# Kernel optimization log

Measured on AMD Instinct MI355X. Metric: run time of the kernel, lower is better.

Reference implementation:

```python
import jax, jax.numpy as jnp
import numpy as np

DIM = 1024
NUM_HEADS = 16
HEAD_DIM = DIM // NUM_HEADS
B, L = 4, 2048


def setup_inputs() -> dict:
    key = jax.random.key(0)
    ks = jax.random.split(key, 9)
    s = 0.02
    return {
        "x": jax.random.normal(ks[0], (B, L, DIM), jnp.float32),
        "Wq": jax.random.normal(ks[1], (DIM, DIM), jnp.float32) * s,
        "bq": jax.random.normal(ks[2], (DIM,), jnp.float32) * s,
        "Wk": jax.random.normal(ks[3], (DIM, DIM), jnp.float32) * s,
        "bk": jax.random.normal(ks[4], (DIM,), jnp.float32) * s,
        "Wv": jax.random.normal(ks[5], (DIM, DIM), jnp.float32) * s,
        "bv": jax.random.normal(ks[6], (DIM,), jnp.float32) * s,
        "Wo": jax.random.normal(ks[7], (DIM, DIM), jnp.float32) * s,
        "bo": jax.random.normal(ks[8], (DIM,), jnp.float32) * s,
    }


def _alibi_bias_causal(seq_len, dtype):
    # slopes m_h = 2^(-8h/H), h = 1..H
    h = jnp.arange(1, NUM_HEADS + 1, dtype=jnp.float32)
    slopes = jnp.power(2.0, -8.0 * h / NUM_HEADS)  # [H]
    pos = jnp.arange(seq_len, dtype=jnp.float32)
    rel = jnp.abs(pos[:, None] - pos[None, :])  # [L, L]
    bias = -slopes[:, None, None] * rel[None, :, :]  # [H, L, L]
    causal = pos[:, None] >= pos[None, :]  # lower-triangular True
    bias = jnp.where(causal[None, :, :], bias, -jnp.inf)
    return bias.astype(dtype)  # [H, L, L]


def reference(x, Wq, bq, Wk, bk, Wv, bv, Wo, bo):
    b, l, d = x.shape
    # torch Linear: y = x @ W.T + b
    q = (jnp.einsum('bld,ed->ble', x, Wq) + bq).reshape(b, l, NUM_HEADS, HEAD_DIM).transpose(0, 2, 1, 3)
    k = (jnp.einsum('bld,ed->ble', x, Wk) + bk).reshape(b, l, NUM_HEADS, HEAD_DIM).transpose(0, 2, 1, 3)
    v = (jnp.einsum('bld,ed->ble', x, Wv) + bv).reshape(b, l, NUM_HEADS, HEAD_DIM).transpose(0, 2, 1, 3)

    scale = 1.0 / np.sqrt(HEAD_DIM)
    scores = jnp.einsum('bhqd,bhkd->bhqk', q, k) * scale  # [B,H,L,L]
    scores = scores + _alibi_bias_causal(l, scores.dtype)[None]  # causal -inf inside bias
    attn = jax.nn.softmax(scores, axis=-1)
    out = jnp.einsum('bhqk,bhkd->bhqd', attn, v)  # [B,H,L,hd]
    out = out.transpose(0, 2, 1, 3).reshape(b, l, d)
    return jnp.einsum('bld,ed->ble', out, Wo) + bo
```

## Files before the change

### kernel.cpp

```cpp
#include <hip/hip_runtime.h>
#include <hip/hip_bf16.h>

typedef __bf16 bf16;
typedef __attribute__((ext_vector_type(4))) __bf16 bf16x4;
typedef __attribute__((ext_vector_type(8))) __bf16 bf16x8;
typedef __attribute__((ext_vector_type(4))) float f32x4;

#define MFMA16(a,b,c) __builtin_amdgcn_mfma_f32_16x16x32_bf16((a),(b),(c),0,0,0)

constexpr int BSZ = 4, SEQ = 2048, DIM = 1024, NH = 16, HD = 64;
constexpr long SZ    = (long)BSZ * SEQ * DIM;
constexpr long BSLOT = (long)SEQ * DIM;
constexpr long WSZ   = (long)DIM * DIM;

__device__ inline bf16x8 ld8(const bf16* p) { return *(const bf16x8*)p; }
__device__ inline bf16x8 ld8(const float* p) {
    f32x4 a = *(const f32x4*)p;
    f32x4 b = *(const f32x4*)(p + 4);
    bf16x8 r;
    r[0] = (bf16)a[0]; r[1] = (bf16)a[1]; r[2] = (bf16)a[2]; r[3] = (bf16)a[3];
    r[4] = (bf16)b[0]; r[5] = (bf16)b[1]; r[6] = (bf16)b[2]; r[7] = (bf16)b[3];
    return r;
}

__device__ inline void async16(const bf16* g, bf16* l) {
    __builtin_amdgcn_global_load_lds(
        (const __attribute__((address_space(1))) unsigned int*)g,
        (__attribute__((address_space(3))) unsigned int*)l,
        16, 0, 0);
}

__global__ __launch_bounds__(256) void cvt1(const float* __restrict__ s,
                                            bf16* __restrict__ d, long n) {
    const long i = ((long)blockIdx.x * 256 + threadIdx.x) * 8;
    if (i < n) *(bf16x8*)(d + i) = ld8(s + i);
}
__global__ __launch_bounds__(256) void cvt3(
    const float* __restrict__ s0, const float* __restrict__ s1, const float* __restrict__ s2,
    bf16* __restrict__ d0, bf16* __restrict__ d1, bf16* __restrict__ d2, long n) {
    const float* s = (blockIdx.z == 0) ? s0 : ((blockIdx.z == 1) ? s1 : s2);
    bf16* d        = (blockIdx.z == 0) ? d0 : ((blockIdx.z == 1) ? d1 : d2);
    const long i = ((long)blockIdx.x * 256 + threadIdx.x) * 8;
    if (i < n) *(bf16x8*)(d + i) = ld8(s + i);
}

template <typename CT>
__global__ __launch_bounds__(256) void gemm_bb(
    const bf16* __restrict__ A,
    const bf16* __restrict__ W0, const bf16* __restrict__ W1, const bf16* __restrict__ W2,
    const float* __restrict__ b0, const float* __restrict__ b1, const float* __restrict__ b2,
    CT* __restrict__ C0, CT* __restrict__ C1, CT* __restrict__ C2,
    int M, int N, int K)
{
    const int z = blockIdx.z;
    const bf16* W     = (z == 0) ? W0 : ((z == 1) ? W1 : W2);
    const float* bias = (z == 0) ? b0 : ((z == 1) ? b1 : b2);
    CT* C             = (z == 0) ? C0 : ((z == 1) ? C1 : C2);

    __shared__ __align__(16) bf16 As[128][32];
    __shared__ __align__(16) bf16 Bs[128][32];

    const int tid  = threadIdx.x;
    const int lane = tid & 63;
    const int wave = tid >> 6;
    const int l15  = lane & 15;
    const int quad = lane >> 4;

    const int m0 = blockIdx.x * 128;
    const int n0 = blockIdx.y * 128;
    const int wm = (wave >> 1) * 64;
    const int wn = (wave & 1) * 64;

    f32x4 acc[4][4];
#pragma unroll
    for (int i = 0; i < 4; i++)
#pragma unroll
        for (int j = 0; j < 4; j++) acc[i][j] = f32x4{0.f, 0.f, 0.f, 0.f};

    const int r1 = tid >> 2,         c1 = (tid & 3) * 8;
    const int r2 = (tid + 256) >> 2, c2 = ((tid + 256) & 3) * 8;

    for (int k0 = 0; k0 < K; k0 += 32) {
        __syncthreads();
        async16(A + (long)(m0 + r1) * K + k0 + c1, &As[r1][c1]);
        async16(A + (long)(m0 + r2) * K + k0 + c2, &As[r2][c2]);
        async16(W + (long)(n0 + r1) * K + k0 + c1, &Bs[r1][c1]);
        async16(W + (long)(n0 + r2) * K + k0 + c2, &Bs[r2][c2]);
        __syncthreads();

        bf16x8 af[4], bfr[4];
#pragma unroll
        for (int t = 0; t < 4; t++) {
            af[t]  = *(const bf16x8*)&As[wm + t * 16 + l15][quad * 8];
            bfr[t] = *(const bf16x8*)&Bs[wn + t * 16 + l15][quad * 8];
        }
#pragma unroll
        for (int i = 0; i < 4; i++)
#pragma unroll
            for (int j = 0; j < 4; j++)
                acc[i][j] = MFMA16(af[i], bfr[j], acc[i][j]);
    }

#pragma unroll
    for (int j = 0; j < 4; j++) {
        const float bv = bias[n0 + wn + j * 16 + l15];
        const long col = n0 + wn + j * 16 + l15;
#pragma unroll
        for (int i = 0; i < 4; i++) {
            const long row = m0 + wm + i * 16 + quad * 4;
#pragma unroll
            for (int r = 0; r < 4; r++)
                C[(row + r) * N + col] = (CT)(acc[i][j][r] + bv);
        }
    }
}

template <typename AT, typename CT>
__global__ __launch_bounds__(256) void gemm_bt(
    const AT* __restrict__ A,
    const float* __restrict__ W0, const float* __restrict__ W1, const float* __restrict__ W2,
    const float* __restrict__ b0, const float* __restrict__ b1, const float* __restrict__ b2,
    CT* __restrict__ C0, CT* __restrict__ C1, CT* __restrict__ C2,
    int M, int N, int K)
{
    const int z = blockIdx.z;
    const float* W    = (z == 0) ? W0 : ((z == 1) ? W1 : W2);
    const float* bias = (z == 0) ? b0 : ((z == 1) ? b1 : b2);
    CT* C             = (z == 0) ? C0 : ((z == 1) ? C1 : C2);

    __shared__ __align__(16) bf16 As[128][32];
    __shared__ __align__(16) bf16 Bs[128][32];

    const int tid  = threadIdx.x;
    const int lane = tid & 63;
    const int wave = tid >> 6;
    const int l15  = lane & 15;
    const int quad = lane >> 4;

    const int m0 = blockIdx.x * 128;
    const int n0 = blockIdx.y * 128;
    const int wm = (wave >> 1) * 64;
    const int wn = (wave & 1) * 64;

    f32x4 acc[4][4];
#pragma unroll
    for (int i = 0; i < 4; i++)
#pragma unroll
        for (int j = 0; j < 4; j++) acc[i][j] = f32x4{0.f, 0.f, 0.f, 0.f};

    const int r1 = tid >> 2,         c1 = (tid & 3) * 8;
    const int r2 = (tid + 256) >> 2, c2 = ((tid + 256) & 3) * 8;

    for (int k0 = 0; k0 < K; k0 += 32) {
        __syncthreads();
        *(bf16x8*)&As[r1][c1] = ld8(A + (long)(m0 + r1) * K + k0 + c1);
        *(bf16x8*)&As[r2][c2] = ld8(A + (long)(m0 + r2) * K + k0 + c2);
        *(bf16x8*)&Bs[r1][c1] = ld8(W + (long)(n0 + r1) * K + k0 + c1);
        *(bf16x8*)&Bs[r2][c2] = ld8(W + (long)(n0 + r2) * K + k0 + c2);
        __syncthreads();

        bf16x8 af[4], bfr[4];
#pragma unroll
        for (int t = 0; t < 4; t++) {
            af[t]  = *(const bf16x8*)&As[wm + t * 16 + l15][quad * 8];
            bfr[t] = *(const bf16x8*)&Bs[wn + t * 16 + l15][quad * 8];
        }
#pragma unroll
        for (int i = 0; i < 4; i++)
#pragma unroll
            for (int j = 0; j < 4; j++)
                acc[i][j] = MFMA16(af[i], bfr[j], acc[i][j]);
    }

#pragma unroll
    for (int j = 0; j < 4; j++) {
        const float bv = bias[n0 + wn + j * 16 + l15];
        const long col = n0 + wn + j * 16 + l15;
#pragma unroll
        for (int i = 0; i < 4; i++) {
            const long row = m0 + wm + i * 16 + quad * 4;
#pragma unroll
            for (int r = 0; r < 4; r++)
                C[(row + r) * N + col] = (CT)(acc[i][j][r] + bv);
        }
    }
}

__global__ __launch_bounds__(256, 4) void attn(
    const bf16* __restrict__ Kw, const bf16* __restrict__ Vw,
    bf16* __restrict__ QOw)
{
    const int z  = blockIdx.x;
    const int bh = blockIdx.y;
    const int b = bh >> 4, h = bh & 15;
    const int qtA = z, qtB = 31 - z;
    const int tid = threadIdx.x, wave = tid >> 6, lane = tid & 63;
    const int l15 = lane & 15, quad = lane >> 4;

    __shared__ __align__(16) bf16 Vt[2][64][72];
    __shared__ __align__(16) bf16 Pl[4][16][72];
    __shared__ __align__(16) bf16 Kt[2][64][64];

    const long base = (long)b * SEQ * DIM + h * HD;
    const int q0A = qtA * 64 + wave * 16;
    const int q0B = qtB * 64 + wave * 16;

    bf16x8 qA0, qA1, qB0, qB1;
    {
        const bf16* pA = QOw + base + (long)(q0A + l15) * DIM + quad * 8;
        qA0 = *(const bf16x8*)pA; qA1 = *(const bf16x8*)(pA + 32);
        const bf16* pB = QOw + base + (long)(q0B + l15) * DIM + quad * 8;
        qB0 = *(const bf16x8*)pB; qB1 = *(const bf16x8*)(pB + 32);
    }

    constexpr float LOG2E = 1.4426950408889634f;
    const float slope = exp2f(-0.5f * (float)(h + 1));
    const float c1 = 0.125f * LOG2E;
    const float ns = slope * LOG2E;
    const float MC = 16.0f * LOG2E;

    float lrA = 0.f, lrB = 0.f;
    f32x4 oA[4], oB[4];
#pragma unroll
    for (int d = 0; d < 4; d++) { oA[d] = f32x4{0,0,0,0}; oB[d] = f32x4{0,0,0,0}; }

    auto stageV = [&](int kt, int bi) {
#pragma unroll
        for (int t = 0; t < 2; t++) {
            const int s = tid + 256 * t;
            const int key = s >> 3, dg8 = (s & 7) * 8;
            bf16x8 v = *(const bf16x8*)(Vw + base + (long)(kt * 64 + key) * DIM + dg8);
            const int col = key ^ dg8;
#pragma unroll
            for (int i = 0; i < 8; i++) Vt[bi][dg8 + i][col] = v[i];
        }
    };

    auto stageK = [&](int kt, int bi) {
#pragma unroll
        for (int t = 0; t < 2; t++) {
            const int s = tid + 256 * t;
            const int r = s >> 3, u = s & 7;
            const int gc = (u ^ (r & 7)) * 8;
            async16(Kw + base + (long)(kt * 64 + r) * DIM + gc, &Kt[bi][r][u * 8]);
        }
    };

    stageK(0, 0);
    stageV(0, 0);
    __syncthreads();

    const int klq = quad * 4;
    const int qlB = wave * 16 + l15;
    const int kc0 = (quad ^ (l15 & 7)) * 8;

    for (int kt = 0; kt <= qtB; kt++) {
        const int bi = kt & 1;
        if (kt < qtB) { stageK(kt + 1, bi ^ 1); stageV(kt + 1, bi ^ 1); }
        const bool dual = (kt <= qtA);

        f32x4 sB[4], sA[4];
#pragma unroll
        for (int nt = 0; nt < 4; nt++) {
            const int row = nt * 16 + l15;
            bf16x8 k0 = *(const bf16x8*)&Kt[bi][row][kc0];
            bf16x8 k1 = *(const bf16x8*)&Kt[bi][row][kc0 ^ 32];
            f32x4 a = f32x4{0,0,0,0};
            a = MFMA16(k0, qB0, a); a = MFMA16(k1, qB1, a);
            sB[nt] = a;
            if (dual) {
                f32x4 c = f32x4{0,0,0,0};
                c = MFMA16(k0, qA0, c); c = MFMA16(k1, qA1, c);
                sA[nt] = c;
            }
        }

        {
            const float t0 = fmaf(ns, (float)(kt * 64 + klq - q0B - l15), -MC);
            const bool diag = (kt == qtB);
#pragma unroll
            for (int nt = 0; nt < 4; nt++) {
                const float bn = fmaf(ns, (float)(16 * nt), t0);
                bf16x4 p4;
#pragma unroll
                for (int r = 0; r < 4; r++) {
                    float arg = fmaf(sB[nt][r], c1, fmaf(ns, (float)r, bn));
                    if (diag && (nt * 16 + klq + r > qlB)) arg = -1e30f;
                    const float p = exp2f(arg);
                    lrB += p;
                    p4[r] = (bf16)p;
                }
                *(bf16x4*)&Pl[wave][l15][nt * 16 + klq] = p4;
            }
            bf16x8 p0 = *(const bf16x8*)&Pl[wave][l15][quad * 8];
            bf16x8 p1 = *(const bf16x8*)&Pl[wave][l15][32 + quad * 8];
#pragma unroll
            for (int dt = 0; dt < 4; dt++) {
                const int d = dt * 16 + l15;
                const int c0 = (quad * 8) ^ (d & 56);
                bf16x8 v0 = *(const bf16x8*)&Vt[bi][d][c0];
                bf16x8 v1 = *(const bf16x8*)&Vt[bi][d][c0 ^ 32];
                oB[dt] = MFMA16(p0, v0, oB[dt]);
                oB[dt] = MFMA16(p1, v1, oB[dt]);
            }
        }

        if (dual) {
            const float t0 = fmaf(ns, (float)(kt * 64 + klq - q0A - l15), -MC);
            const bool diag = (kt == qtA);
#pragma unroll
            for (int nt = 0; nt < 4; nt++) {
                const float bn = fmaf(ns, (float)(16 * nt), t0);
                bf16x4 p4;
#pragma unroll
                for (int r = 0; r < 4; r++) {
                    float arg = fmaf(sA[nt][r], c1, fmaf(ns, (float)r, bn));
                    if (diag && (nt * 16 + klq + r > qlB)) arg = -1e30f;
                    const float p = exp2f(arg);
                    lrA += p;
                    p4[r] = (bf16)p;
                }
                *(bf16x4*)&Pl[wave][l15][nt * 16 + klq] = p4;
            }
            bf16x8 p0 = *(const bf16x8*)&Pl[wave][l15][quad * 8];
            bf16x8 p1 = *(const bf16x8*)&Pl[wave][l15][32 + quad * 8];
#pragma unroll
            for (int dt = 0; dt < 4; dt++) {
                const int d = dt * 16 + l15;
                const int c0 = (quad * 8) ^ (d & 56);
                bf16x8 v0 = *(const bf16x8*)&Vt[bi][d][c0];
                bf16x8 v1 = *(const bf16x8*)&Vt[bi][d][c0 ^ 32];
                oA[dt] = MFMA16(p0, v0, oA[dt]);
                oA[dt] = MFMA16(p1, v1, oA[dt]);
            }
        }
        __syncthreads();
    }

    lrB += __shfl_xor(lrB, 16, 64); lrB += __shfl_xor(lrB, 32, 64);
    lrA += __shfl_xor(lrA, 16, 64); lrA += __shfl_xor(lrA, 32, 64);
#pragma unroll
    for (int r = 0; r < 4; r++) {
        const float ivB = 1.0f / __shfl(lrB, quad * 4 + r, 64);
        const float ivA = 1.0f / __shfl(lrA, quad * 4 + r, 64);
        const long rwB = q0B + quad * 4 + r;
        const long rwA = q0A + quad * 4 + r;
#pragma unroll
        for (int dt = 0; dt < 4; dt++) {
            QOw[base + rwB * DIM + dt * 16 + l15] = (bf16)(oB[dt][r] * ivB);
            QOw[base + rwA * DIM + dt * 16 + l15] = (bf16)(oA[dt][r] * ivA);
        }
    }
}

extern "C" void kernel_launch(void* const* d_in, const int* in_sizes, int n_in,
                              void* d_out, int out_size, void* d_ws, size_t ws_size,
                              hipStream_t stream)
{
    const float* x  = (const float*)d_in[0];
    const float* Wq = (const float*)d_in[1];
    const float* bq = (const float*)d_in[2];
    const float* Wk = (const float*)d_in[3];
    const float* bk = (const float*)d_in[4];
    const float* Wv = (const float*)d_in[5];
    const float* bv = (const float*)d_in[6];
    const float* Wo = (const float*)d_in[7];
    const float* bo = (const float*)d_in[8];
    float* out = (float*)d_out;

    dim3 blk(256, 1, 1);

    if (ws_size >= (size_t)SZ * sizeof(bf16)) {
        bf16* xb  = (bf16*)d_out;
        bf16* Wqb = xb + SZ;
        bf16* Wkb = Wqb + WSZ;
        bf16* Wvb = Wkb + WSZ;
        bf16* Qb  = (bf16*)d_ws;
        bf16* Kb  = (bf16*)d_in[0];
        bf16* Vb  = Kb + SZ;
        bf16* Wob = Kb;

        cvt1<<<dim3(4096, 1, 1), blk, 0, stream>>>(x, xb, SZ);
        cvt3<<<dim3(512, 1, 3), blk, 0, stream>>>(Wq, Wk, Wv, Wqb, Wkb, Wvb, WSZ);

        dim3 g1(64, 8, 3);
        gemm_bb<bf16><<<g1, blk, 0, stream>>>(xb, Wqb, Wkb, Wvb, bq, bk, bv,
                                              Qb, Kb, Vb, BSZ * SEQ, DIM, DIM);
        dim3 g2(16, BSZ * NH, 1);
        attn<<<g2, blk, 0, stream>>>(Kb, Vb, Qb);

        cvt1<<<dim3(512, 1, 1), blk, 0, stream>>>(Wo, Wob, WSZ);

        dim3 g3(64, 8, 1);
        gemm_bb<float><<<g3, blk, 0, stream>>>(Qb, Wob, Wob, Wob, bo, bo, bo,
                                               out, out, out, BSZ * SEQ, DIM, DIM);
    } else {
        bf16* outB = (bf16*)d_out;
        float* xm = const_cast<float*>(x);
        bf16* x0a = (bf16*)xm;
        bf16* x0b = x0a + BSLOT;
        bf16* x1a = (bf16*)(xm + BSLOT);

        bf16* Qs[4] = { outB + 2 * BSLOT, x0a, x0a, x0a };
        bf16* Ks[4] = { outB + 3 * BSLOT, x0b, x0b, x0b };
        bf16* Vs[4] = { outB + 4 * BSLOT, outB + 6 * BSLOT, x1a, x1a };

        dim3 gqkv(SEQ / 128, DIM / 128, 3);
        dim3 gattn(16, NH, 1);
        dim3 gproj(SEQ / 128, DIM / 128, 1);

        for (int b = 0; b < 4; b++) {
            gemm_bt<float, bf16><<<gqkv, blk, 0, stream>>>(x + b * BSLOT, Wq, Wk, Wv,
                                                           bq, bk, bv,
                                                           Qs[b], Ks[b], Vs[b], SEQ, DIM, DIM);
            attn<<<gattn, blk, 0, stream>>>(Ks[b], Vs[b], Qs[b]);
            gemm_bt<bf16, float><<<gproj, blk, 0, stream>>>(Qs[b], Wo, Wo, Wo, bo, bo, bo,
                                                            out + b * BSLOT, out + b * BSLOT,
                                                            out + b * BSLOT, SEQ, DIM, DIM);
        }
    }
}
```

Measured before the change: 316.2 us.

## Double-buffer GEMM LDS tiles and overlap V prefetch with softmax in attention

The projection GEMM gets double-buffered LDS tiles, so the next K-slice is loaded asynchronously while MFMAs run on the current one, and only one barrier is paid per iteration. In the attention kernel, V for the next tile is loaded into registers early and written to LDS after the softmax and PV work. Both query tiles' softmax is computed before their PV MFMAs, using separate P buffers, to give the scheduler more independent work. The cost is more LDS and register pressure, which may lower occupancy.

```diff
diff --git a/kernel.cpp b/kernel.cpp
--- a/kernel.cpp
+++ b/kernel.cpp
@@ -57,8 +57,8 @@
     const float* bias = (z == 0) ? b0 : ((z == 1) ? b1 : b2);
     CT* C             = (z == 0) ? C0 : ((z == 1) ? C1 : C2);
 
-    __shared__ __align__(16) bf16 As[128][32];
-    __shared__ __align__(16) bf16 Bs[128][32];
+    __shared__ __align__(16) bf16 As[2][128][32];
+    __shared__ __align__(16) bf16 Bs[2][128][32];
 
     const int tid  = threadIdx.x;
     const int lane = tid & 63;
@@ -80,25 +80,36 @@
     const int r1 = tid >> 2,         c1 = (tid & 3) * 8;
     const int r2 = (tid + 256) >> 2, c2 = ((tid + 256) & 3) * 8;
 
-    for (int k0 = 0; k0 < K; k0 += 32) {
-        __syncthreads();
-        async16(A + (long)(m0 + r1) * K + k0 + c1, &As[r1][c1]);
-        async16(A + (long)(m0 + r2) * K + k0 + c2, &As[r2][c2]);
-        async16(W + (long)(n0 + r1) * K + k0 + c1, &Bs[r1][c1]);
-        async16(W + (long)(n0 + r2) * K + k0 + c2, &Bs[r2][c2]);
-        __syncthreads();
+    async16(A + (long)(m0 + r1) * K + c1, &As[0][r1][c1]);
+    async16(A + (long)(m0 + r2) * K + c2, &As[0][r2][c2]);
+    async16(W + (long)(n0 + r1) * K + c1, &Bs[0][r1][c1]);
+    async16(W + (long)(n0 + r2) * K + c2, &Bs[0][r2][c2]);
+    __syncthreads();
+
+    const int NT = K >> 5;
+    for (int t = 0; t < NT; t++) {
+        const int cur = t & 1;
+        if (t + 1 < NT) {
+            const int k0 = (t + 1) * 32;
+            async16(A + (long)(m0 + r1) * K + k0 + c1, &As[cur ^ 1][r1][c1]);
+            async16(A + (long)(m0 + r2) * K + k0 + c2, &As[cur ^ 1][r2][c2]);
+            async16(W + (long)(n0 + r1) * K + k0 + c1, &Bs[cur ^ 1][r1][c1]);
+            async16(W + (long)(n0 + r2) * K + k0 + c2, &Bs[cur ^ 1][r2][c2]);
+        }
 
         bf16x8 af[4], bfr[4];
 #pragma unroll
-        for (int t = 0; t < 4; t++) {
-            af[t]  = *(const bf16x8*)&As[wm + t * 16 + l15][quad * 8];
-            bfr[t] = *(const bf16x8*)&Bs[wn + t * 16 + l15][quad * 8];
+        for (int t4 = 0; t4 < 4; t4++) {
+            af[t4]  = *(const bf16x8*)&As[cur][wm + t4 * 16 + l15][quad * 8];
+            bfr[t4] = *(const bf16x8*)&Bs[cur][wn + t4 * 16 + l15][quad * 8];
         }
 #pragma unroll
         for (int i = 0; i < 4; i++)
 #pragma unroll
             for (int j = 0; j < 4; j++)
                 acc[i][j] = MFMA16(af[i], bfr[j], acc[i][j]);
+
+        __syncthreads();
     }
 
 #pragma unroll
@@ -198,8 +209,8 @@
     const int l15 = lane & 15, quad = lane >> 4;
 
     __shared__ __align__(16) bf16 Vt[2][64][72];
-    __shared__ __align__(16) bf16 Pl[4][16][72];
     __shared__ __align__(16) bf16 Kt[2][64][64];
+    __shared__ __align__(16) bf16 Pl[2][4][16][72];
 
     const long base = (long)b * SEQ * DIM + h * HD;
     const int q0A = qtA * 64 + wave * 16;
@@ -224,17 +235,9 @@
 #pragma unroll
     for (int d = 0; d < 4; d++) { oA[d] = f32x4{0,0,0,0}; oB[d] = f32x4{0,0,0,0}; }
 
-    auto stageV = [&](int kt, int bi) {
-#pragma unroll
-        for (int t = 0; t < 2; t++) {
-            const int s = tid + 256 * t;
-            const int key = s >> 3, dg8 = (s & 7) * 8;
-            bf16x8 v = *(const bf16x8*)(Vw + base + (long)(kt * 64 + key) * DIM + dg8);
-            const int col = key ^ dg8;
-#pragma unroll
-            for (int i = 0; i < 8; i++) Vt[bi][dg8 + i][col] = v[i];
-        }
-    };
+    const int sk0 = tid >> 3,         sd0 = (tid & 7) * 8;
+    const int sk1 = (tid + 256) >> 3, sd1 = ((tid + 256) & 7) * 8;
+    const int vc0 = sk0 ^ sd0,        vc1 = sk1 ^ sd1;
 
     auto stageK = [&](int kt, int bi) {
 #pragma unroll
@@ -247,7 +250,14 @@
     };
 
     stageK(0, 0);
-    stageV(0, 0);
+    {
+        bf16x8 v0 = *(const bf16x8*)(Vw + base + (long)sk0 * DIM + sd0);
+        bf16x8 v1 = *(const bf16x8*)(Vw + base + (long)sk1 * DIM + sd1);
+#pragma unroll
+        for (int i = 0; i < 8; i++) Vt[0][sd0 + i][vc0] = v0[i];
+#pragma unroll
+        for (int i = 0; i < 8; i++) Vt[0][sd1 + i][vc1] = v1[i];
+    }
     __syncthreads();
 
     const int klq = quad * 4;
@@ -256,8 +266,15 @@
 
     for (int kt = 0; kt <= qtB; kt++) {
         const int bi = kt & 1;
-        if (kt < qtB) { stageK(kt + 1, bi ^ 1); stageV(kt + 1, bi ^ 1); }
+        const bool more = (kt < qtB);
         const bool dual = (kt <= qtA);
+
+        bf16x8 vn0, vn1;
+        if (more) {
+            stageK(kt + 1, bi ^ 1);
+            vn0 = *(const bf16x8*)(Vw + base + (long)((kt + 1) * 64 + sk0) * DIM + sd0);
+            vn1 = *(const bf16x8*)(Vw + base + (long)((kt + 1) * 64 + sk1) * DIM + sd1);
+        }
 
         f32x4 sB[4], sA[4];
 #pragma unroll
@@ -290,10 +307,37 @@
                     lrB += p;
                     p4[r] = (bf16)p;
                 }
-                *(bf16x4*)&Pl[wave][l15][nt * 16 + klq] = p4;
+                *(bf16x4*)&Pl[0][wave][l15][nt * 16 + klq] = p4;
             }
-            bf16x8 p0 = *(const bf16x8*)&Pl[wave][l15][quad * 8];
-            bf16x8 p1 = *(const bf16x8*)&Pl[wave][l15][32 + quad * 8];
+        }
+
+        if (dual) {
+            const float t0 = fmaf(ns, (float)(kt * 64 + klq - q0A - l15), -MC);
+            const bool diag = (kt == qtA);
+#pragma unroll
+            for (int nt = 0; nt < 4; nt++) {
+                const float bn = fmaf(ns, (float)(16 * nt), t0);
+                bf16x4 p4;
+#pragma unroll
+                for (int r = 0; r < 4; r++) {
+                    float arg = fmaf(sA[nt][r], c1, fmaf(ns, (float)r, bn));
+                    if (diag && (nt * 16 + klq + r > qlB)) arg = -1e30f;
+                    const float p = exp2f(arg);
+                    lrA += p;
+                    p4[r] = (bf16)p;
+                }
+                *(bf16x4*)&Pl[1][wave][l15][nt * 16 + klq] = p4;
+            }
+        } else if (more) {
+#pragma unroll
+            for (int i = 0; i < 8; i++) Vt[bi ^ 1][sd0 + i][vc0] = vn0[i];
+#pragma unroll
+            for (int i = 0; i < 8; i++) Vt[bi ^ 1][sd1 + i][vc1] = vn1[i];
+        }
+
+        {
+            bf16x8 p0 = *(const bf16x8*)&Pl[0][wave][l15][quad * 8];
+            bf16x8 p1 = *(const bf16x8*)&Pl[0][wave][l15][32 + quad * 8];
 #pragma unroll
             for (int dt = 0; dt < 4; dt++) {
                 const int d = dt * 16 + l15;
@@ -306,24 +350,8 @@
         }
 
         if (dual) {
-            const float t0 = fmaf(ns, (float)(kt * 64 + klq - q0A - l15), -MC);
-            const bool diag = (kt == qtA);
-#pragma unroll
-            for (int nt = 0; nt < 4; nt++) {
-                const float bn = fmaf(ns, (float)(16 * nt), t0);
-                bf16x4 p4;
-#pragma unroll
-                for (int r = 0; r < 4; r++) {
-                    float arg = fmaf(sA[nt][r], c1, fmaf(ns, (float)r, bn));
-                    if (diag && (nt * 16 + klq + r > qlB)) arg = -1e30f;
-                    const float p = exp2f(arg);
-                    lrA += p;
-                    p4[r] = (bf16)p;
-                }
-                *(bf16x4*)&Pl[wave][l15][nt * 16 + klq] = p4;
-            }
-            bf16x8 p0 = *(const bf16x8*)&Pl[wave][l15][quad * 8];
-            bf16x8 p1 = *(const bf16x8*)&Pl[wave][l15][32 + quad * 8];
+            bf16x8 p0 = *(const bf16x8*)&Pl[1][wave][l15][quad * 8];
+            bf16x8 p1 = *(const bf16x8*)&Pl[1][wave][l15][32 + quad * 8];
 #pragma unroll
             for (int dt = 0; dt < 4; dt++) {
                 const int d = dt * 16 + l15;
@@ -333,6 +361,10 @@
                 oA[dt] = MFMA16(p0, v0, oA[dt]);
                 oA[dt] = MFMA16(p1, v1, oA[dt]);
             }
+#pragma unroll
+            for (int i = 0; i < 8; i++) Vt[bi ^ 1][sd0 + i][vc0] = vn0[i];
+#pragma unroll
+            for (int i = 0; i < 8; i++) Vt[bi ^ 1][sd1 + i][vc1] = vn1[i];
         }
         __syncthreads();
     }
```

Result: faster. 303.0 us (-4.2%).
